# Kernel optimization log

Hardware: AMD Instinct MI355X
Metric: run time of the kernel (lower is better)

Reference implementation:

```python
import jax, jax.numpy as jnp
import numpy as np

B, T = 256, 4096
L = 128          # shapelet_length
K = 128          # num_shapelets
K_TOP = 5


def setup_inputs() -> dict:
    key = jax.random.key(0)
    kx, ks = jax.random.split(key)
    x = jax.random.normal(kx, (B, T), dtype=jnp.float32)
    shapelets = jax.random.normal(ks, (K, L), dtype=jnp.float32) * 0.1
    return {"x": x, "shapelets": shapelets}


def reference(x, shapelets):
    # x: [B, T], shapelets: [K, L]
    N = x.shape[1] - L + 1  # number of sliding windows
    # Gather overlapping windows: x_win [B, N, L]
    idx = jnp.arange(N)[:, None] + jnp.arange(L)[None, :]
    x_win = x[:, idx]
    # Per-window mean removal
    x_norm = x_win - jnp.mean(x_win, axis=2, keepdims=True)
    # Per-shapelet mean removal
    s_norm = shapelets - jnp.mean(shapelets, axis=1, keepdims=True)
    # Correlation: [B, N, K]
    corr = jnp.einsum('bnl,kl->bnk', x_norm, s_norm)
    k_val = min(K_TOP, N)
    # top-k over window dim N -> move N to last axis
    topk_vals, _ = jax.lax.top_k(jnp.transpose(corr, (0, 2, 1)), k_val)  # [B, K, k]
    p1 = topk_vals[:, :, 0]
    p2 = topk_vals[:, :, 1] if k_val >= 2 else p1
    p_mean = jnp.mean(topk_vals, axis=2)
    dominance = jax.nn.relu(p1 - p2)
    return jnp.concatenate([p1, p_mean, p2, dominance], axis=1)  # [B, 4K]
```

## Files before the change

### kernel.cpp

```cpp
#include <hip/hip_runtime.h>

#define T_LEN 4096
#define N_WIN 3969
#define K_SH  128
#define L_SH  128
#define B_SZ  256

#define SSTR  136
#define XSTR  4360

typedef __attribute__((ext_vector_type(8))) __bf16 bf16x8;
typedef __attribute__((ext_vector_type(4))) float f32x4;
typedef _Float16 h2 __attribute__((ext_vector_type(2)));

__device__ __forceinline__ unsigned short f2bf(float f) {
    union { float f; unsigned int u; } c; c.f = f;
    unsigned int u = c.u + 0x7fff + ((c.u >> 16) & 1u);
    return (unsigned short)(u >> 16);
}
__device__ __forceinline__ unsigned int pack2(unsigned short lo, unsigned short hi) {
    return (unsigned int)lo | ((unsigned int)hi << 16);
}

__device__ __forceinline__ h2 max2(h2 a, h2 b) { return __builtin_elementwise_max(a, b); }
__device__ __forceinline__ h2 min2(h2 a, h2 b) { return __builtin_elementwise_min(a, b); }
__device__ __forceinline__ h2 cvt2(float lo, float hi) {
    return __builtin_bit_cast(h2, __builtin_amdgcn_cvt_pkrtz(lo, hi));
}
__device__ __forceinline__ void ce2(h2& hi, h2& lo) {
    const h2 m = max2(hi, lo);
    lo = min2(hi, lo);
    hi = m;
}
__device__ __forceinline__ void sort4_2(h2& a, h2& b, h2& c, h2& d) {
    ce2(a, b); ce2(c, d); ce2(a, c); ce2(b, d); ce2(b, c);
}
__device__ __forceinline__ void merge44_top5_2(h2 a0, h2 a1, h2 a2, h2 a3,
                                               h2 b0, h2 b1, h2 b2, h2 b3,
                                               h2& r0, h2& r1, h2& r2, h2& r3, h2& r4) {
    ce2(a0, b0); ce2(a2, b2); ce2(b0, a2);
    ce2(a1, b1); ce2(a3, b3); ce2(b1, a3);
    r0 = a0;
    r1 = a1; r2 = b0; ce2(r1, r2);
    r3 = b1; r4 = a2; ce2(r3, r4);
}
__device__ __forceinline__ void merge55_2(h2& r0, h2& r1, h2& r2, h2& r3, h2& r4,
                                          h2 s0, h2 s1, h2 s2, h2 s3, h2 s4) {
    const h2 m00 = min2(r0, s0);
    const h2 m10 = min2(r1, s0), m01 = min2(r0, s1);
    const h2 m20 = min2(r2, s0), m11 = min2(r1, s1), m02 = min2(r0, s2);
    const h2 m30 = min2(r3, s0), m21 = min2(r2, s1), m12 = min2(r1, s2), m03 = min2(r0, s3);
    const h2 n0 = max2(r0, s0);
    const h2 n1 = max2(max2(r1, s1), m00);
    const h2 n2 = max2(max2(r2, s2), max2(m10, m01));
    const h2 n3 = max2(max2(max2(r3, s3), m20), max2(m11, m02));
    const h2 n4 = max2(max2(max2(r4, s4), max2(m30, m03)), max2(m21, m12));
    r0 = n0; r1 = n1; r2 = n2; r3 = n3; r4 = n4;
}
__device__ __forceinline__ void insert1_2(h2 v, h2* rt) {
    h2 b = max2(rt[4], v); h2 m;
    m = max2(rt[3], b);     b     = min2(rt[3], b);     rt[3] = m;
    m = max2(rt[2], rt[3]); rt[3] = min2(rt[2], rt[3]); rt[2] = m;
    m = max2(rt[1], rt[2]); rt[2] = min2(rt[1], rt[2]); rt[1] = m;
    m = max2(rt[0], rt[1]); rt[1] = min2(rt[0], rt[1]); rt[0] = m;
    rt[4] = b;
}
__device__ __forceinline__ void select32(const f32x4* acc0, const f32x4* acc1, h2* rt) {
    h2 p[16];
    #pragma unroll
    for (int m = 0; m < 4; ++m)
        #pragma unroll
        for (int i = 0; i < 4; ++i)
            p[4 * m + i] = cvt2(acc0[m][i], acc1[m][i]);
    sort4_2(p[0], p[1], p[2],  p[3]);
    sort4_2(p[4], p[5], p[6],  p[7]);
    sort4_2(p[8], p[9], p[10], p[11]);
    sort4_2(p[12], p[13], p[14], p[15]);
    h2 u0, u1, u2, u3, u4, v0, v1, v2, v3, v4;
    merge44_top5_2(p[0], p[1], p[2],  p[3],  p[4],  p[5],  p[6],  p[7],  u0, u1, u2, u3, u4);
    merge44_top5_2(p[8], p[9], p[10], p[11], p[12], p[13], p[14], p[15], v0, v1, v2, v3, v4);
    merge55_2(u0, u1, u2, u3, u4, v0, v1, v2, v3, v4);
    merge55_2(rt[0], rt[1], rt[2], rt[3], rt[4], u0, u1, u2, u3, u4);
}

__global__ __launch_bounds__(1024, 4)
void shapelet_fused_kernel(const float* __restrict__ x,
                           const float* __restrict__ s,
                           float* __restrict__ out) {
    __shared__ __align__(16) unsigned short ldsS[K_SH * SSTR];
    __shared__ __align__(16) unsigned short ldsX[8 * XSTR];

    const int t    = threadIdx.x;
    const int lane = t & 63;
    const int w    = t >> 6;
    const int r    = lane & 15;
    const int q    = lane >> 4;
    const int c7   = lane & 7;
    const int ub   = (lane >> 3) & 1;
    const int g    = w >> 3;
    const int w7   = w & 7;
    const int mh   = w7 >> 2;
    const int wp   = w7 & 3;
    const int mtb  = 4 * mh;
    const int b    = blockIdx.x;

    {
        const int k = t >> 3, e8 = t & 7;
        const float4* srow = (const float4*)(s + k * L_SH + e8 * 16);
        float4 v[4];
        float sum = 0.0f;
        #pragma unroll
        for (int j = 0; j < 4; ++j) {
            v[j] = srow[j];
            sum += (v[j].x + v[j].y) + (v[j].z + v[j].w);
        }
        sum += __shfl_xor(sum, 1);
        sum += __shfl_xor(sum, 2);
        sum += __shfl_xor(sum, 4);
        const float mean = sum * (1.0f / 128.0f);
        uint4* dst = (uint4*)((char*)ldsS + k * (SSTR * 2) + e8 * 32);
        #pragma unroll
        for (int j = 0; j < 2; ++j) {
            uint4 o;
            o.x = pack2(f2bf(v[2*j].x - mean),   f2bf(v[2*j].y - mean));
            o.y = pack2(f2bf(v[2*j].z - mean),   f2bf(v[2*j].w - mean));
            o.z = pack2(f2bf(v[2*j+1].x - mean), f2bf(v[2*j+1].y - mean));
            o.w = pack2(f2bf(v[2*j+1].z - mean), f2bf(v[2*j+1].w - mean));
            dst[j] = o;
        }
        if (e8 == 7) *(uint4*)((char*)ldsS + k * (SSTR * 2) + 256) = make_uint4(0,0,0,0);
    }

    {
        const float* __restrict__ xb = x + (size_t)b * T_LEN;
        const int a = (t ^ (t >> 3)) & 7;
        for (int i = (t >> 3); i < XSTR / 8; i += 128) {
            const int p0 = 8 * i;
            float xv[16];
            if (p0 + 16 <= T_LEN) {
                const float4* sp = (const float4*)(xb + p0);
                #pragma unroll
                for (int j = 0; j < 4; ++j) *(float4*)(xv + 4 * j) = sp[j];
            } else {
                #pragma unroll
                for (int j = 0; j < 16; ++j) {
                    const int gi = p0 + j;
                    xv[j] = (gi < T_LEN) ? xb[gi] : 0.0f;
                }
            }
            unsigned short bv[16];
            #pragma unroll
            for (int j = 0; j < 16; ++j) bv[j] = f2bf(xv[j]);
            uint4 o;
            o.x = pack2(bv[a],     bv[a + 1]);
            o.y = pack2(bv[a + 2], bv[a + 3]);
            o.z = pack2(bv[a + 4], bv[a + 5]);
            o.w = pack2(bv[a + 6], bv[a + 7]);
            *(uint4*)((char*)ldsX + a * (XSTR * 2) + 2 * p0) = o;
        }
    }
    __syncthreads();

    bf16x8 bfr[2][4];
    #pragma unroll
    for (int kk = 0; kk < 2; ++kk)
        #pragma unroll
        for (int c = 0; c < 4; ++c)
            bfr[kk][c] = __builtin_bit_cast(bf16x8, *(const uint4*)(
                (const char*)ldsS + ((2 * wp + kk) * 16 + r) * (SSTR * 2) + 64 * c + 16 * q));

    h2 rt[5];
    #pragma unroll
    for (int i = 0; i < 5; ++i) rt[i] = __builtin_bit_cast(h2, 0xFC00FC00u);

    {
        const int ph = (w >> 2) & 3;
        if (ph == 1)      __builtin_amdgcn_s_sleep(8);
        else if (ph == 2) __builtin_amdgcn_s_sleep(16);
        else if (ph == 3) __builtin_amdgcn_s_sleep(24);
    }

    const char* xp = (const char*)ldsX + c7 * (XSTR * 2) + 16 * q + 16 * ub + 32 * mtb
                   + g * 256;

    const f32x4 ZCC = (f32x4){0.f, 0.f, 0.f, 0.f};

#define TILE_STEP                                                               \
    {                                                                           \
        bf16x8 afr[10];                                                         \
        _Pragma("unroll")                                                       \
        for (int j = 0; j < 10; ++j)                                            \
            afr[j] = __builtin_bit_cast(bf16x8, *(const uint4*)(xp + 32 * j));  \
        xp += 512;                                                              \
        f32x4 acc0[4], acc1[4];                                                 \
        __builtin_amdgcn_s_setprio(1);                                          \
        _Pragma("unroll")                                                       \
        for (int m = 0; m < 4; ++m) {                                           \
            acc0[m] = __builtin_amdgcn_mfma_f32_16x16x32_bf16(afr[m], bfr[0][0], ZCC, 0, 0, 0); \
            acc1[m] = __builtin_amdgcn_mfma_f32_16x16x32_bf16(afr[m], bfr[1][0], ZCC, 0, 0, 0); \
        }                                                                       \
        _Pragma("unroll")                                                       \
        for (int c = 1; c < 4; ++c) {                                           \
            _Pragma("unroll")                                                   \
            for (int m = 0; m < 4; ++m) {                                       \
                acc0[m] = __builtin_amdgcn_mfma_f32_16x16x32_bf16(afr[m + 2*c], bfr[0][c], acc0[m], 0, 0, 0); \
                acc1[m] = __builtin_amdgcn_mfma_f32_16x16x32_bf16(afr[m + 2*c], bfr[1][c], acc1[m], 0, 0, 0); \
            }                                                                   \
        }                                                                       \
        __builtin_amdgcn_s_setprio(0);                                          \
        select32(acc0, acc1, rt);                                               \
    }

    for (int st = 0; st < 15; ++st) { TILE_STEP }
    if (g == 0) { TILE_STEP }
#undef TILE_STEP

    if (g == 1 && mh == 0) {
        f32x4 e0 = (f32x4){0.f, 0.f, 0.f, 0.f};
        f32x4 e1 = (f32x4){0.f, 0.f, 0.f, 0.f};
        const char* eb = (const char*)ldsX + c7 * (XSTR * 2) + 7936 + 16 * q + 16 * ub;
        #pragma unroll
        for (int c = 0; c < 4; ++c) {
            const bf16x8 af = __builtin_bit_cast(bf16x8, *(const uint4*)(eb + 64 * c));
            e0 = __builtin_amdgcn_mfma_f32_16x16x32_bf16(af, bfr[0][c], e0, 0, 0, 0);
            e1 = __builtin_amdgcn_mfma_f32_16x16x32_bf16(af, bfr[1][c], e1, 0, 0, 0);
        }
        if (q == 0) insert1_2(cvt2(e0[0], e1[0]), rt);
    }

    #pragma unroll
    for (int mask = 16; mask <= 32; mask <<= 1) {
        h2 sv[5];
        #pragma unroll
        for (int i = 0; i < 5; ++i)
            sv[i] = __builtin_bit_cast(h2, __shfl_xor(__builtin_bit_cast(int, rt[i]), mask));
        merge55_2(rt[0], rt[1], rt[2], rt[3], rt[4], sv[0], sv[1], sv[2], sv[3], sv[4]);
    }

    __syncthreads();
    unsigned int* pbuf = (unsigned int*)ldsS;
    if ((g != 0 || mh != 0) && q == 0) {
        const int reg = (g * 2 + mh) - 1;
        unsigned int* p = pbuf + ((reg * 64) + wp * 16 + r) * 5;
        #pragma unroll
        for (int i = 0; i < 5; ++i) p[i] = __builtin_bit_cast(unsigned int, rt[i]);
    }
    __syncthreads();
    if (g == 0 && mh == 0 && q == 0) {
        #pragma unroll
        for (int reg = 0; reg < 3; ++reg) {
            const unsigned int* p = pbuf + ((reg * 64) + wp * 16 + r) * 5;
            h2 sv[5];
            #pragma unroll
            for (int i = 0; i < 5; ++i) sv[i] = __builtin_bit_cast(h2, p[i]);
            merge55_2(rt[0], rt[1], rt[2], rt[3], rt[4], sv[0], sv[1], sv[2], sv[3], sv[4]);
        }

        const float A0 = (float)rt[0][0], A1 = (float)rt[1][0], A2 = (float)rt[2][0],
                    A3 = (float)rt[3][0], A4 = (float)rt[4][0];
        const float B0 = (float)rt[0][1], B1 = (float)rt[1][1], B2 = (float)rt[2][1],
                    B3 = (float)rt[3][1], B4 = (float)rt[4][1];
        float* ob = out + (size_t)b * (4 * K_SH);
        const int ksA = 32 * wp + r, ksB = ksA + 16;
        const float mA = (((A0 + A1) + (A2 + A3)) + A4) * 0.2f;
        const float mB = (((B0 + B1) + (B2 + B3)) + B4) * 0.2f;
        ob[ksA]           = A0;
        ob[K_SH + ksA]    = mA;
        ob[2*K_SH + ksA]  = A1;
        ob[3*K_SH + ksA]  = fmaxf(A0 - A1, 0.0f);
        ob[ksB]           = B0;
        ob[K_SH + ksB]    = mB;
        ob[2*K_SH + ksB]  = B1;
        ob[3*K_SH + ksB]  = fmaxf(B0 - B1, 0.0f);
    }
}

extern "C" void kernel_launch(void* const* d_in, const int* in_sizes, int n_in,
                              void* d_out, int out_size, void* d_ws, size_t ws_size,
                              hipStream_t stream) {
    const float* x = (const float*)d_in[0];
    const float* s = (const float*)d_in[1];
    float* out = (float*)d_out;
    shapelet_fused_kernel<<<B_SZ, 1024, 0, stream>>>(x, s, out);
}
```

Baseline: 93.12 us.

## Split each batch row into eight window chunks with a separate top-k merge kernel

Adds a two-kernel path. The first kernel launches 8 blocks of 256 threads per batch row, each covering 512 windows; each block builds its bf16 shapelet fragments directly from global memory and writes per-shapelet top-5 lists to workspace. A second small kernel merges the eight partial lists and computes the outputs. The aim is better occupancy and load balance than one 1024-thread block per row, at the cost of redundant shapelet loads, a workspace round trip and an extra launch. The old fused kernel also loses its staggered s_sleep and setprio hints.

```diff
diff --git a/kernel.cpp b/kernel.cpp
--- a/kernel.cpp
+++ b/kernel.cpp
@@ -8,6 +8,9 @@
 
 #define SSTR  136
 #define XSTR  4360
+
+#define XSTR_E 648
+#define W_EIGHTH 512
 
 typedef __attribute__((ext_vector_type(8))) __bf16 bf16x8;
 typedef __attribute__((ext_vector_type(4))) float f32x4;
@@ -81,6 +84,191 @@
     merge44_top5_2(p[8], p[9], p[10], p[11], p[12], p[13], p[14], p[15], v0, v1, v2, v3, v4);
     merge55_2(u0, u1, u2, u3, u4, v0, v1, v2, v3, v4);
     merge55_2(rt[0], rt[1], rt[2], rt[3], rt[4], u0, u1, u2, u3, u4);
+}
+
+__global__ __launch_bounds__(256, 8)
+void shapelet_oct_kernel(const float* __restrict__ x,
+                         const float* __restrict__ s,
+                         unsigned int* __restrict__ wslists) {
+    __shared__ __align__(16) unsigned short ldsX[8 * XSTR_E];
+    __shared__ float ldsMean[K_SH];
+
+    const int t    = threadIdx.x;
+    const int lane = t & 63;
+    const int w    = t >> 6;
+    const int r    = lane & 15;
+    const int q    = lane >> 4;
+    const int c7   = lane & 7;
+    const int ub   = (lane >> 3) & 1;
+    const int bid  = blockIdx.x;
+    const int b    = bid >> 3;
+    const int qt   = bid & 7;
+    const int qbase = qt << 9;
+
+    {
+        const int row = t >> 1, half = t & 1;
+        const float4* sp = (const float4*)(s + row * L_SH + half * 64);
+        float sum = 0.0f;
+        #pragma unroll
+        for (int j = 0; j < 16; ++j) {
+            const float4 v = sp[j];
+            sum += (v.x + v.y) + (v.z + v.w);
+        }
+        sum += __shfl_xor(sum, 1);
+        if (!half) ldsMean[row] = sum * (1.0f / 128.0f);
+    }
+
+    {
+        const float* __restrict__ xb = x + (size_t)b * T_LEN + qbase;
+        const int lim = T_LEN - qbase;
+        const int a = t & 7;
+        for (int i = (t >> 3); i < XSTR_E / 8; i += 32) {
+            const int p0 = 8 * i;
+            float xv[16];
+            if (p0 + 16 <= lim) {
+                const float4* sp = (const float4*)(xb + p0);
+                #pragma unroll
+                for (int j = 0; j < 4; ++j) *(float4*)(xv + 4 * j) = sp[j];
+            } else {
+                #pragma unroll
+                for (int j = 0; j < 16; ++j) {
+                    const int gi = p0 + j;
+                    xv[j] = (gi < lim) ? xb[gi] : 0.0f;
+                }
+            }
+            unsigned short bv[16];
+            #pragma unroll
+            for (int j = 0; j < 16; ++j) bv[j] = f2bf(xv[j]);
+            uint4 o;
+            o.x = pack2(bv[a],     bv[a + 1]);
+            o.y = pack2(bv[a + 2], bv[a + 3]);
+            o.z = pack2(bv[a + 4], bv[a + 5]);
+            o.w = pack2(bv[a + 6], bv[a + 7]);
+            *(uint4*)((char*)ldsX + a * (XSTR_E * 2) + 2 * p0) = o;
+        }
+    }
+    __syncthreads();
+
+    bf16x8 bfr[2][4];
+    #pragma unroll
+    for (int kk = 0; kk < 2; ++kk) {
+        const int krow = (2 * w + kk) * 16 + r;
+        const float mean = ldsMean[krow];
+        #pragma unroll
+        for (int c = 0; c < 4; ++c) {
+            const float4* sp = (const float4*)(s + krow * L_SH + 32 * c + 8 * q);
+            const float4 v0 = sp[0], v1 = sp[1];
+            uint4 o;
+            o.x = pack2(f2bf(v0.x - mean), f2bf(v0.y - mean));
+            o.y = pack2(f2bf(v0.z - mean), f2bf(v0.w - mean));
+            o.z = pack2(f2bf(v1.x - mean), f2bf(v1.y - mean));
+            o.w = pack2(f2bf(v1.z - mean), f2bf(v1.w - mean));
+            bfr[kk][c] = __builtin_bit_cast(bf16x8, o);
+        }
+    }
+
+    h2 rt[5];
+    #pragma unroll
+    for (int i = 0; i < 5; ++i) rt[i] = __builtin_bit_cast(h2, 0xFC00FC00u);
+
+    const char* xp = (const char*)ldsX + c7 * (XSTR_E * 2) + 16 * q + 16 * ub;
+
+    const f32x4 ZCC = (f32x4){0.f, 0.f, 0.f, 0.f};
+
+#define TILE_STEP                                                               \
+    {                                                                           \
+        bf16x8 afr[10];                                                         \
+        _Pragma("unroll")                                                       \
+        for (int j = 0; j < 10; ++j)                                            \
+            afr[j] = __builtin_bit_cast(bf16x8, *(const uint4*)(xp + 32 * j));  \
+        xp += 128;                                                              \
+        f32x4 acc0[4], acc1[4];                                                 \
+        _Pragma("unroll")                                                       \
+        for (int m = 0; m < 4; ++m) {                                           \
+            acc0[m] = __builtin_amdgcn_mfma_f32_16x16x32_bf16(afr[m], bfr[0][0], ZCC, 0, 0, 0); \
+            acc1[m] = __builtin_amdgcn_mfma_f32_16x16x32_bf16(afr[m], bfr[1][0], ZCC, 0, 0, 0); \
+        }                                                                       \
+        _Pragma("unroll")                                                       \
+        for (int c = 1; c < 4; ++c) {                                           \
+            _Pragma("unroll")                                                   \
+            for (int m = 0; m < 4; ++m) {                                       \
+                acc0[m] = __builtin_amdgcn_mfma_f32_16x16x32_bf16(afr[m + 2*c], bfr[0][c], acc0[m], 0, 0, 0); \
+                acc1[m] = __builtin_amdgcn_mfma_f32_16x16x32_bf16(afr[m + 2*c], bfr[1][c], acc1[m], 0, 0, 0); \
+            }                                                                   \
+        }                                                                       \
+        select32(acc0, acc1, rt);                                               \
+    }
+
+    const int nst = (qt == 7) ? 6 : 8;
+    for (int st = 0; st < nst; ++st) { TILE_STEP }
+#undef TILE_STEP
+
+    if (qt == 7) {
+        f32x4 e0 = (f32x4){0.f, 0.f, 0.f, 0.f};
+        f32x4 e1 = (f32x4){0.f, 0.f, 0.f, 0.f};
+        const char* eb = (const char*)ldsX + c7 * (XSTR_E * 2) + 768 + 16 * q + 16 * ub;
+        #pragma unroll
+        for (int c = 0; c < 4; ++c) {
+            const bf16x8 af = __builtin_bit_cast(bf16x8, *(const uint4*)(eb + 64 * c));
+            e0 = __builtin_amdgcn_mfma_f32_16x16x32_bf16(af, bfr[0][c], e0, 0, 0, 0);
+            e1 = __builtin_amdgcn_mfma_f32_16x16x32_bf16(af, bfr[1][c], e1, 0, 0, 0);
+        }
+        if (q == 0) insert1_2(cvt2(e0[0], e1[0]), rt);
+    }
+
+    #pragma unroll
+    for (int mask = 16; mask <= 32; mask <<= 1) {
+        h2 sv[5];
+        #pragma unroll
+        for (int i = 0; i < 5; ++i)
+            sv[i] = __builtin_bit_cast(h2, __shfl_xor(__builtin_bit_cast(int, rt[i]), mask));
+        merge55_2(rt[0], rt[1], rt[2], rt[3], rt[4], sv[0], sv[1], sv[2], sv[3], sv[4]);
+    }
+
+    if (q == 0) {
+        unsigned int* p = wslists + ((size_t)(b * 8 + qt) * 64 + (w * 16 + r)) * 5;
+        #pragma unroll
+        for (int i = 0; i < 5; ++i) p[i] = __builtin_bit_cast(unsigned int, rt[i]);
+    }
+}
+
+__global__ __launch_bounds__(256)
+void shapelet_merge8_kernel(const unsigned int* __restrict__ wslists,
+                            float* __restrict__ out) {
+    const int j = blockIdx.x * 256 + threadIdx.x;
+    const int b = j >> 6;
+    const int pair = j & 63;
+    h2 rt[5];
+    {
+        const unsigned int* p = wslists + ((size_t)(b * 8 + 0) * 64 + pair) * 5;
+        #pragma unroll
+        for (int i = 0; i < 5; ++i) rt[i] = __builtin_bit_cast(h2, p[i]);
+    }
+    #pragma unroll
+    for (int e = 1; e < 8; ++e) {
+        const unsigned int* p = wslists + ((size_t)(b * 8 + e) * 64 + pair) * 5;
+        h2 sv[5];
+        #pragma unroll
+        for (int i = 0; i < 5; ++i) sv[i] = __builtin_bit_cast(h2, p[i]);
+        merge55_2(rt[0], rt[1], rt[2], rt[3], rt[4], sv[0], sv[1], sv[2], sv[3], sv[4]);
+    }
+
+    const float A0 = (float)rt[0][0], A1 = (float)rt[1][0], A2 = (float)rt[2][0],
+                A3 = (float)rt[3][0], A4 = (float)rt[4][0];
+    const float B0 = (float)rt[0][1], B1 = (float)rt[1][1], B2 = (float)rt[2][1],
+                B3 = (float)rt[3][1], B4 = (float)rt[4][1];
+    float* ob = out + (size_t)b * (4 * K_SH);
+    const int ksA = 32 * (pair >> 4) + (pair & 15), ksB = ksA + 16;
+    const float mA = (((A0 + A1) + (A2 + A3)) + A4) * 0.2f;
+    const float mB = (((B0 + B1) + (B2 + B3)) + B4) * 0.2f;
+    ob[ksA]           = A0;
+    ob[K_SH + ksA]    = mA;
+    ob[2*K_SH + ksA]  = A1;
+    ob[3*K_SH + ksA]  = fmaxf(A0 - A1, 0.0f);
+    ob[ksB]           = B0;
+    ob[K_SH + ksB]    = mB;
+    ob[2*K_SH + ksB]  = B1;
+    ob[3*K_SH + ksB]  = fmaxf(B0 - B1, 0.0f);
 }
 
 __global__ __launch_bounds__(1024, 4)
@@ -130,7 +318,6 @@
         }
         if (e8 == 7) *(uint4*)((char*)ldsS + k * (SSTR * 2) + 256) = make_uint4(0,0,0,0);
     }
-
     {
         const float* __restrict__ xb = x + (size_t)b * T_LEN;
         const int a = (t ^ (t >> 3)) & 7;
@@ -173,16 +360,8 @@
     #pragma unroll
     for (int i = 0; i < 5; ++i) rt[i] = __builtin_bit_cast(h2, 0xFC00FC00u);
 
-    {
-        const int ph = (w >> 2) & 3;
-        if (ph == 1)      __builtin_amdgcn_s_sleep(8);
-        else if (ph == 2) __builtin_amdgcn_s_sleep(16);
-        else if (ph == 3) __builtin_amdgcn_s_sleep(24);
-    }
-
     const char* xp = (const char*)ldsX + c7 * (XSTR * 2) + 16 * q + 16 * ub + 32 * mtb
                    + g * 256;
-
     const f32x4 ZCC = (f32x4){0.f, 0.f, 0.f, 0.f};
 
 #define TILE_STEP                                                               \
@@ -193,7 +372,6 @@
             afr[j] = __builtin_bit_cast(bf16x8, *(const uint4*)(xp + 32 * j));  \
         xp += 512;                                                              \
         f32x4 acc0[4], acc1[4];                                                 \
-        __builtin_amdgcn_s_setprio(1);                                          \
         _Pragma("unroll")                                                       \
         for (int m = 0; m < 4; ++m) {                                           \
             acc0[m] = __builtin_amdgcn_mfma_f32_16x16x32_bf16(afr[m], bfr[0][0], ZCC, 0, 0, 0); \
@@ -207,7 +385,6 @@
                 acc1[m] = __builtin_amdgcn_mfma_f32_16x16x32_bf16(afr[m + 2*c], bfr[1][c], acc1[m], 0, 0, 0); \
             }                                                                   \
         }                                                                       \
-        __builtin_amdgcn_s_setprio(0);                                          \
         select32(acc0, acc1, rt);                                               \
     }
 
@@ -255,7 +432,6 @@
             for (int i = 0; i < 5; ++i) sv[i] = __builtin_bit_cast(h2, p[i]);
             merge55_2(rt[0], rt[1], rt[2], rt[3], rt[4], sv[0], sv[1], sv[2], sv[3], sv[4]);
         }
-
         const float A0 = (float)rt[0][0], A1 = (float)rt[1][0], A2 = (float)rt[2][0],
                     A3 = (float)rt[3][0], A4 = (float)rt[4][0];
         const float B0 = (float)rt[0][1], B1 = (float)rt[1][1], B2 = (float)rt[2][1],
@@ -281,5 +457,12 @@
     const float* x = (const float*)d_in[0];
     const float* s = (const float*)d_in[1];
     float* out = (float*)d_out;
-    shapelet_fused_kernel<<<B_SZ, 1024, 0, stream>>>(x, s, out);
-}
+    const size_t ws_needed = (size_t)B_SZ * 8 * 64 * 5 * sizeof(unsigned int);
+    if (d_ws != nullptr && ws_size >= ws_needed) {
+        unsigned int* wslists = (unsigned int*)d_ws;
+        shapelet_oct_kernel<<<8 * B_SZ, 256, 0, stream>>>(x, s, wslists);
+        shapelet_merge8_kernel<<<64, 256, 0, stream>>>(wslists, out);
+    } else {
+        shapelet_fused_kernel<<<B_SZ, 1024, 0, stream>>>(x, s, out);
+    }
+}
```

Result: slower. 148.1 us (+59.0%).

## Halve block to 512 threads, each wave covering 64 shapelets

Applied to the files above, without the earlier changes.

The block shrinks from 16 to 8 waves. Each wave now computes two 32-shapelet groups (rtP/rtQ) from the same loaded A fragments, which doubles reuse of the x-window LDS reads per MFMA. It also removes the staggered s_sleep start and the s_setprio hints. In exchange each wave holds more registers (16 B fragments and two top-5 sets), and there are fewer waves per CU to hide latency.

```diff
diff --git a/kernel.cpp b/kernel.cpp
--- a/kernel.cpp
+++ b/kernel.cpp
@@ -83,10 +83,10 @@
     merge55_2(rt[0], rt[1], rt[2], rt[3], rt[4], u0, u1, u2, u3, u4);
 }
 
-__global__ __launch_bounds__(1024, 4)
-void shapelet_fused_kernel(const float* __restrict__ x,
-                           const float* __restrict__ s,
-                           float* __restrict__ out) {
+__global__ __launch_bounds__(512, 2)
+void shapelet_fused8_kernel(const float* __restrict__ x,
+                            const float* __restrict__ s,
+                            float* __restrict__ out) {
     __shared__ __align__(16) unsigned short ldsS[K_SH * SSTR];
     __shared__ __align__(16) unsigned short ldsX[8 * XSTR];
 
@@ -97,30 +97,28 @@
     const int q    = lane >> 4;
     const int c7   = lane & 7;
     const int ub   = (lane >> 3) & 1;
-    const int g    = w >> 3;
-    const int w7   = w & 7;
-    const int mh   = w7 >> 2;
-    const int wp   = w7 & 3;
+    const int g    = w >> 2;
+    const int mh   = (w >> 1) & 1;
+    const int wp   = w & 1;
     const int mtb  = 4 * mh;
     const int b    = blockIdx.x;
 
     {
-        const int k = t >> 3, e8 = t & 7;
-        const float4* srow = (const float4*)(s + k * L_SH + e8 * 16);
-        float4 v[4];
+        const int k = t >> 2, e4 = t & 3;
+        const float4* srow = (const float4*)(s + k * L_SH + e4 * 32);
+        float4 v[8];
         float sum = 0.0f;
         #pragma unroll
-        for (int j = 0; j < 4; ++j) {
+        for (int j = 0; j < 8; ++j) {
             v[j] = srow[j];
             sum += (v[j].x + v[j].y) + (v[j].z + v[j].w);
         }
         sum += __shfl_xor(sum, 1);
         sum += __shfl_xor(sum, 2);
-        sum += __shfl_xor(sum, 4);
         const float mean = sum * (1.0f / 128.0f);
-        uint4* dst = (uint4*)((char*)ldsS + k * (SSTR * 2) + e8 * 32);
-        #pragma unroll
-        for (int j = 0; j < 2; ++j) {
+        uint4* dst = (uint4*)((char*)ldsS + k * (SSTR * 2) + e4 * 64);
+        #pragma unroll
+        for (int j = 0; j < 4; ++j) {
             uint4 o;
             o.x = pack2(f2bf(v[2*j].x - mean),   f2bf(v[2*j].y - mean));
             o.y = pack2(f2bf(v[2*j].z - mean),   f2bf(v[2*j].w - mean));
@@ -128,13 +126,13 @@
             o.w = pack2(f2bf(v[2*j+1].z - mean), f2bf(v[2*j+1].w - mean));
             dst[j] = o;
         }
-        if (e8 == 7) *(uint4*)((char*)ldsS + k * (SSTR * 2) + 256) = make_uint4(0,0,0,0);
+        if (e4 == 3) *(uint4*)((char*)ldsS + k * (SSTR * 2) + 256) = make_uint4(0,0,0,0);
     }
 
     {
         const float* __restrict__ xb = x + (size_t)b * T_LEN;
         const int a = (t ^ (t >> 3)) & 7;
-        for (int i = (t >> 3); i < XSTR / 8; i += 128) {
+        for (int i = (t >> 3); i < XSTR / 8; i += 64) {
             const int p0 = 8 * i;
             float xv[16];
             if (p0 + 16 <= T_LEN) {
@@ -161,23 +159,19 @@
     }
     __syncthreads();
 
-    bf16x8 bfr[2][4];
+    bf16x8 bfr[4][4];
     #pragma unroll
-    for (int kk = 0; kk < 2; ++kk)
+    for (int kt = 0; kt < 4; ++kt)
         #pragma unroll
         for (int c = 0; c < 4; ++c)
-            bfr[kk][c] = __builtin_bit_cast(bf16x8, *(const uint4*)(
-                (const char*)ldsS + ((2 * wp + kk) * 16 + r) * (SSTR * 2) + 64 * c + 16 * q));
-
-    h2 rt[5];
+            bfr[kt][c] = __builtin_bit_cast(bf16x8, *(const uint4*)(
+                (const char*)ldsS + ((64 * wp + 16 * kt + r)) * (SSTR * 2) + 64 * c + 16 * q));
+
+    h2 rtP[5], rtQ[5];
     #pragma unroll
-    for (int i = 0; i < 5; ++i) rt[i] = __builtin_bit_cast(h2, 0xFC00FC00u);
-
-    {
-        const int ph = (w >> 2) & 3;
-        if (ph == 1)      __builtin_amdgcn_s_sleep(8);
-        else if (ph == 2) __builtin_amdgcn_s_sleep(16);
-        else if (ph == 3) __builtin_amdgcn_s_sleep(24);
+    for (int i = 0; i < 5; ++i) {
+        rtP[i] = __builtin_bit_cast(h2, 0xFC00FC00u);
+        rtQ[i] = __builtin_bit_cast(h2, 0xFC00FC00u);
     }
 
     const char* xp = (const char*)ldsX + c7 * (XSTR * 2) + 16 * q + 16 * ub + 32 * mtb
@@ -193,7 +187,6 @@
             afr[j] = __builtin_bit_cast(bf16x8, *(const uint4*)(xp + 32 * j));  \
         xp += 512;                                                              \
         f32x4 acc0[4], acc1[4];                                                 \
-        __builtin_amdgcn_s_setprio(1);                                          \
         _Pragma("unroll")                                                       \
         for (int m = 0; m < 4; ++m) {                                           \
             acc0[m] = __builtin_amdgcn_mfma_f32_16x16x32_bf16(afr[m], bfr[0][0], ZCC, 0, 0, 0); \
@@ -207,71 +200,104 @@
                 acc1[m] = __builtin_amdgcn_mfma_f32_16x16x32_bf16(afr[m + 2*c], bfr[1][c], acc1[m], 0, 0, 0); \
             }                                                                   \
         }                                                                       \
-        __builtin_amdgcn_s_setprio(0);                                          \
-        select32(acc0, acc1, rt);                                               \
-    }
-
-    for (int st = 0; st < 15; ++st) { TILE_STEP }
-    if (g == 0) { TILE_STEP }
+        select32(acc0, acc1, rtP);                                              \
+        _Pragma("unroll")                                                       \
+        for (int m = 0; m < 4; ++m) {                                           \
+            acc0[m] = __builtin_amdgcn_mfma_f32_16x16x32_bf16(afr[m], bfr[2][0], ZCC, 0, 0, 0); \
+            acc1[m] = __builtin_amdgcn_mfma_f32_16x16x32_bf16(afr[m], bfr[3][0], ZCC, 0, 0, 0); \
+        }                                                                       \
+        _Pragma("unroll")                                                       \
+        for (int c = 1; c < 4; ++c) {                                           \
+            _Pragma("unroll")                                                   \
+            for (int m = 0; m < 4; ++m) {                                       \
+                acc0[m] = __builtin_amdgcn_mfma_f32_16x16x32_bf16(afr[m + 2*c], bfr[2][c], acc0[m], 0, 0, 0); \
+                acc1[m] = __builtin_amdgcn_mfma_f32_16x16x32_bf16(afr[m + 2*c], bfr[3][c], acc1[m], 0, 0, 0); \
+            }                                                                   \
+        }                                                                       \
+        select32(acc0, acc1, rtQ);                                              \
+    }
+
+    const int nst = (g == 0) ? 16 : 15;
+    for (int st = 0; st < nst; ++st) { TILE_STEP }
 #undef TILE_STEP
 
     if (g == 1 && mh == 0) {
-        f32x4 e0 = (f32x4){0.f, 0.f, 0.f, 0.f};
-        f32x4 e1 = (f32x4){0.f, 0.f, 0.f, 0.f};
+        f32x4 e[4];
+        #pragma unroll
+        for (int kt = 0; kt < 4; ++kt) e[kt] = (f32x4){0.f, 0.f, 0.f, 0.f};
         const char* eb = (const char*)ldsX + c7 * (XSTR * 2) + 7936 + 16 * q + 16 * ub;
         #pragma unroll
         for (int c = 0; c < 4; ++c) {
             const bf16x8 af = __builtin_bit_cast(bf16x8, *(const uint4*)(eb + 64 * c));
-            e0 = __builtin_amdgcn_mfma_f32_16x16x32_bf16(af, bfr[0][c], e0, 0, 0, 0);
-            e1 = __builtin_amdgcn_mfma_f32_16x16x32_bf16(af, bfr[1][c], e1, 0, 0, 0);
-        }
-        if (q == 0) insert1_2(cvt2(e0[0], e1[0]), rt);
+            #pragma unroll
+            for (int kt = 0; kt < 4; ++kt)
+                e[kt] = __builtin_amdgcn_mfma_f32_16x16x32_bf16(af, bfr[kt][c], e[kt], 0, 0, 0);
+        }
+        if (q == 0) {
+            insert1_2(cvt2(e[0][0], e[1][0]), rtP);
+            insert1_2(cvt2(e[2][0], e[3][0]), rtQ);
+        }
     }
 
     #pragma unroll
     for (int mask = 16; mask <= 32; mask <<= 1) {
-        h2 sv[5];
-        #pragma unroll
-        for (int i = 0; i < 5; ++i)
-            sv[i] = __builtin_bit_cast(h2, __shfl_xor(__builtin_bit_cast(int, rt[i]), mask));
-        merge55_2(rt[0], rt[1], rt[2], rt[3], rt[4], sv[0], sv[1], sv[2], sv[3], sv[4]);
+        h2 sv[5], sw[5];
+        #pragma unroll
+        for (int i = 0; i < 5; ++i) {
+            sv[i] = __builtin_bit_cast(h2, __shfl_xor(__builtin_bit_cast(int, rtP[i]), mask));
+            sw[i] = __builtin_bit_cast(h2, __shfl_xor(__builtin_bit_cast(int, rtQ[i]), mask));
+        }
+        merge55_2(rtP[0], rtP[1], rtP[2], rtP[3], rtP[4], sv[0], sv[1], sv[2], sv[3], sv[4]);
+        merge55_2(rtQ[0], rtQ[1], rtQ[2], rtQ[3], rtQ[4], sw[0], sw[1], sw[2], sw[3], sw[4]);
     }
 
     __syncthreads();
     unsigned int* pbuf = (unsigned int*)ldsS;
-    if ((g != 0 || mh != 0) && q == 0) {
-        const int reg = (g * 2 + mh) - 1;
-        unsigned int* p = pbuf + ((reg * 64) + wp * 16 + r) * 5;
-        #pragma unroll
-        for (int i = 0; i < 5; ++i) p[i] = __builtin_bit_cast(unsigned int, rt[i]);
+    const int gm = g * 2 + mh;
+    if (gm != 0 && q == 0) {
+        unsigned int* p = pbuf + ((wp * 3 + (gm - 1)) * 16 + r) * 10;
+        #pragma unroll
+        for (int i = 0; i < 5; ++i) {
+            p[i]     = __builtin_bit_cast(unsigned int, rtP[i]);
+            p[5 + i] = __builtin_bit_cast(unsigned int, rtQ[i]);
+        }
     }
     __syncthreads();
-    if (g == 0 && mh == 0 && q == 0) {
+    if (gm == 0 && q == 0) {
         #pragma unroll
         for (int reg = 0; reg < 3; ++reg) {
-            const unsigned int* p = pbuf + ((reg * 64) + wp * 16 + r) * 5;
-            h2 sv[5];
+            const unsigned int* p = pbuf + ((wp * 3 + reg) * 16 + r) * 10;
+            h2 sv[5], sw[5];
             #pragma unroll
-            for (int i = 0; i < 5; ++i) sv[i] = __builtin_bit_cast(h2, p[i]);
-            merge55_2(rt[0], rt[1], rt[2], rt[3], rt[4], sv[0], sv[1], sv[2], sv[3], sv[4]);
-        }
-
-        const float A0 = (float)rt[0][0], A1 = (float)rt[1][0], A2 = (float)rt[2][0],
-                    A3 = (float)rt[3][0], A4 = (float)rt[4][0];
-        const float B0 = (float)rt[0][1], B1 = (float)rt[1][1], B2 = (float)rt[2][1],
-                    B3 = (float)rt[3][1], B4 = (float)rt[4][1];
+            for (int i = 0; i < 5; ++i) {
+                sv[i] = __builtin_bit_cast(h2, p[i]);
+                sw[i] = __builtin_bit_cast(h2, p[5 + i]);
+            }
+            merge55_2(rtP[0], rtP[1], rtP[2], rtP[3], rtP[4], sv[0], sv[1], sv[2], sv[3], sv[4]);
+            merge55_2(rtQ[0], rtQ[1], rtQ[2], rtQ[3], rtQ[4], sw[0], sw[1], sw[2], sw[3], sw[4]);
+        }
+
         float* ob = out + (size_t)b * (4 * K_SH);
-        const int ksA = 32 * wp + r, ksB = ksA + 16;
-        const float mA = (((A0 + A1) + (A2 + A3)) + A4) * 0.2f;
-        const float mB = (((B0 + B1) + (B2 + B3)) + B4) * 0.2f;
-        ob[ksA]           = A0;
-        ob[K_SH + ksA]    = mA;
-        ob[2*K_SH + ksA]  = A1;
-        ob[3*K_SH + ksA]  = fmaxf(A0 - A1, 0.0f);
-        ob[ksB]           = B0;
-        ob[K_SH + ksB]    = mB;
-        ob[2*K_SH + ksB]  = B1;
-        ob[3*K_SH + ksB]  = fmaxf(B0 - B1, 0.0f);
+        const h2* rts[2] = { rtP, rtQ };
+        #pragma unroll
+        for (int setI = 0; setI < 2; ++setI) {
+            const h2* rt = rts[setI];
+            const float A0 = (float)rt[0][0], A1 = (float)rt[1][0], A2 = (float)rt[2][0],
+                        A3 = (float)rt[3][0], A4 = (float)rt[4][0];
+            const float B0 = (float)rt[0][1], B1 = (float)rt[1][1], B2 = (float)rt[2][1],
+                        B3 = (float)rt[3][1], B4 = (float)rt[4][1];
+            const int ksA = 64 * wp + 32 * setI + r, ksB = ksA + 16;
+            const float mA = (((A0 + A1) + (A2 + A3)) + A4) * 0.2f;
+            const float mB = (((B0 + B1) + (B2 + B3)) + B4) * 0.2f;
+            ob[ksA]           = A0;
+            ob[K_SH + ksA]    = mA;
+            ob[2*K_SH + ksA]  = A1;
+            ob[3*K_SH + ksA]  = fmaxf(A0 - A1, 0.0f);
+            ob[ksB]           = B0;
+            ob[K_SH + ksB]    = mB;
+            ob[2*K_SH + ksB]  = B1;
+            ob[3*K_SH + ksB]  = fmaxf(B0 - B1, 0.0f);
+        }
     }
 }
 
@@ -281,5 +307,5 @@
     const float* x = (const float*)d_in[0];
     const float* s = (const float*)d_in[1];
     float* out = (float*)d_out;
-    shapelet_fused_kernel<<<B_SZ, 1024, 0, stream>>>(x, s, out);
-}
+    shapelet_fused8_kernel<<<B_SZ, 512, 0, stream>>>(x, s, out);
+}
```

Measured after the change: 98.23 us. +5.5%, slower.
